# Performance work log

Measured on AMD Instinct MI355X. Metric: run time of the kernel, lower is better.

## Reference

```python
import jax, jax.numpy as jnp
import numpy as np

NUM_NODES = 200000
NUM_EDGES = 300000
NUM_QUERIES = 128
NUM_ENTITIES = 50000
N_DIMS = 256
N_DIMS_SM = 64
STATIC_DIM = 128
STATIC_SM = 32
G_IN = 2 * N_DIMS_SM + STATIC_SM + N_DIMS_SM  # 224


def leaky(x):
    return jnp.where(x > 0, x, 0.01 * x)


def setup_inputs() -> dict:
    key = jax.random.key(0)
    ks = jax.random.split(key, 24)
    W = 0.05  # weight scale to keep logits in a sane range
    inp = {
        'memorized_embedding': jax.random.normal(ks[0], (NUM_NODES, N_DIMS), jnp.float32),
        'node_score': jax.random.uniform(ks[1], (NUM_NODES,), jnp.float32),
        'rel_emb': jax.random.normal(ks[2], (NUM_EDGES, N_DIMS), jnp.float32),
        'query_src_ts_emb': jax.random.normal(ks[3], (NUM_QUERIES, STATIC_DIM), jnp.float32),
        'query_rel_emb': jax.random.normal(ks[4], (NUM_QUERIES, N_DIMS), jnp.float32),
        'eg_idx': jax.random.randint(ks[5], (NUM_EDGES,), 0, NUM_QUERIES, jnp.int32),
        'src_idx': jax.random.randint(ks[6], (NUM_EDGES,), 0, NUM_NODES, jnp.int32),
        'dst_idx': jax.random.randint(ks[7], (NUM_EDGES,), 0, NUM_NODES, jnp.int32),
        'entity_idx': jax.random.randint(ks[8], (NUM_NODES,), 0, NUM_ENTITIES, jnp.int32),
        'W_proj': W * jax.random.normal(ks[9], (N_DIMS, N_DIMS_SM), jnp.float32),
        'b_proj': W * jax.random.normal(ks[10], (N_DIMS_SM,), jnp.float32),
        'W_static': W * jax.random.normal(ks[11], (STATIC_DIM, STATIC_SM), jnp.float32),
        'b_static': W * jax.random.normal(ks[12], (STATIC_SM,), jnp.float32),
        'W_bs': W * jax.random.normal(ks[13], (N_DIMS, N_DIMS), jnp.float32),
        'b_bs': W * jax.random.normal(ks[14], (N_DIMS,), jnp.float32),
        'Wl': W * jax.random.normal(ks[15], (G_IN, N_DIMS_SM), jnp.float32),
        'bl': W * jax.random.normal(ks[16], (N_DIMS_SM,), jnp.float32),
        'Wr': W * jax.random.normal(ks[17], (G_IN, N_DIMS_SM), jnp.float32),
        'br': W * jax.random.normal(ks[18], (N_DIMS_SM,), jnp.float32),
        'Wc': W * jax.random.normal(ks[19], (N_DIMS_SM, N_DIMS_SM), jnp.float32),
        'bc': W * jax.random.normal(ks[20], (N_DIMS_SM,), jnp.float32),
    }
    return inp


def reference(memorized_embedding, node_score, rel_emb, query_src_ts_emb, query_rel_emb,
              eg_idx, src_idx, dst_idx, entity_idx,
              W_proj, b_proj, W_static, b_static, W_bs, b_bs,
              Wl, bl, Wr, br, Wc, bc):
    # one attention-flow step: linear_between_steps -> attention scoring (G) ->
    # per-source-node softmax -> attention propagation -> per-entity aggregation
    emb2 = leaky(memorized_embedding @ W_bs + b_bs)        # [N, d]
    # project all node embeddings once (linear commutes with gather)
    proj_all = emb2 @ W_proj + b_proj                       # [N, d_sm]
    hvi = proj_all[src_idx]                                 # [E, d_sm]
    hvj = proj_all[dst_idx]                                 # [E, d_sm]
    rel = rel_emb @ W_proj + b_proj                         # [E, d_sm]
    # context_dim_red
    qs = query_src_ts_emb @ W_static + b_static             # [B, static_sm]
    qr = query_rel_emb @ W_proj + b_proj                    # [B, d_sm]
    qs_e = qs[eg_idx]                                       # [E, static_sm]
    qr_e = qr[eg_idx]                                       # [E, d_sm]
    left = jnp.concatenate([hvi, rel, qs_e, qr_e], axis=-1)   # [E, G_IN]
    right = jnp.concatenate([hvj, rel, qs_e, qr_e], axis=-1)  # [E, G_IN]
    # G: sum(leaky(left W_l) * ((leaky(right W_r)) W_c))
    lh = leaky(left @ Wl + bl)                              # [E, d_sm]
    rh = leaky(right @ Wr + br) @ Wc + bc                   # [E, d_sm]
    logits = jnp.sum(lh * rh, axis=-1)                      # [E]
    # transition probability: softmax over outgoing edges of each source node
    seg_max = jax.ops.segment_max(logits, src_idx, num_segments=NUM_NODES)
    ex = jnp.exp(logits - seg_max[src_idx])
    denom = jax.ops.segment_sum(ex, src_idx, num_segments=NUM_NODES)
    trans = ex / denom[src_idx]
    # propagate node attention along edges (node_score_aggregation='sum')
    new_node_score = jax.ops.segment_sum(trans * node_score[src_idx], dst_idx,
                                         num_segments=NUM_NODES)
    # _aggregate_op_entity: sparse COO matmul == segment_sum over entity groups
    entity_att_score = jax.ops.segment_sum(new_node_score, entity_idx,
                                           num_segments=NUM_ENTITIES)
    return entity_att_score
```

## Files before the change

kernel.cpp:

```cpp
#include <hip/hip_runtime.h>
#include <hip/hip_bf16.h>

#define N_NODES 200000
#define N_EDGES 300000
#define N_Q     128
#define N_ENT   50000
#define D       256
#define DSM     64
#define SDIM    128
#define SSM     32

typedef __attribute__((ext_vector_type(8))) short bf16x8;
typedef __attribute__((ext_vector_type(4))) float f32x4;

__device__ __forceinline__ float leaky(float x){ return x > 0.f ? x : 0.01f*x; }

__device__ __forceinline__ unsigned short f2bf(float f){
  __hip_bfloat16 h = __float2bfloat16(f);
  return *reinterpret_cast<unsigned short*>(&h);
}
__device__ __forceinline__ unsigned pk2bf(float a, float b){
  float2 t; t.x = a; t.y = b;
  __hip_bfloat162 h = __float22bfloat162_rn(t);
  return *reinterpret_cast<unsigned*>(&h);
}
__device__ __forceinline__ float bf2f(unsigned short h){
  return __uint_as_float(((unsigned)h) << 16);
}

__device__ __forceinline__ void dev_pack(const float* __restrict__ src,
                                         unsigned short* __restrict__ dst,
                                         int K, int N, int id, int total){
  if (id >= total) return;
  int lane = id & 63, fb = id >> 6;
  int KB = K >> 5;
  int kb = fb % KB, nb = fb / KB;
  int k0 = kb*32 + ((lane>>4)<<3);
  int n  = nb*16 + (lane & 15);
  #pragma unroll
  for (int i = 0; i < 8; ++i) dst[(size_t)id*8 + i] = f2bf(src[(size_t)(k0+i)*N + n]);
}

__global__ void k_setup1(float* out, float* denom,
                         const float* __restrict__ Wp, const float* __restrict__ Wl,
                         const float* __restrict__ Wr, float* Wnlr, float* Wrlr,
                         const float* __restrict__ bp, float* cv,
                         const float* __restrict__ qsrc, const float* __restrict__ Ws,
                         const float* __restrict__ bs, const float* __restrict__ qrel,
                         float* qs, float* qr,
                         const float* __restrict__ Wbs, unsigned short* Wbs_pk,
                         const float* __restrict__ Wc, unsigned short* Wc_pk){
  int b = blockIdx.x, tid = threadIdx.x;
  if (b < 782){
    int id = b*256 + tid;
    if (id < N_ENT) out[id] = 0.f;
    if (id < N_NODES) denom[id] = 0.f;
  } else if (b < 1038){
    int id = (b-782)*256 + tid;
    int m = id >> 14, rem = id & 16383, k = rem >> 6, c = rem & 63;
    const float* Wsrc = (m & 1) ? Wr : Wl;
    int roff = (m >> 1) * 64;
    float s = 0.f;
    for (int i = 0; i < 64; ++i) s += Wp[k*64+i] * Wsrc[(roff+i)*64 + c];
    float* o = (m >> 1) ? Wrlr : Wnlr;
    o[k*128 + (m&1)*64 + c] = s;
  } else if (b == 1038){
    int m = tid >> 6, c = tid & 63;
    const float* Wsrc = (m & 1) ? Wr : Wl;
    int roff = (m >> 1) * 64;
    float s = 0.f;
    for (int i = 0; i < 64; ++i) s += bp[i] * Wsrc[(roff+i)*64 + c];
    cv[tid] = s;
  } else if (b < 1087){
    int id = (b-1039)*256 + tid;
    if (id < N_Q*SSM){
      int q = id >> 5, i = id & 31;
      float s = bs[i];
      for (int j = 0; j < SDIM; ++j) s += qsrc[q*SDIM+j] * Ws[j*SSM+i];
      qs[id] = s;
    } else {
      int id2 = id - N_Q*SSM;
      int q = id2 >> 6, i = id2 & 63;
      float s = bp[i];
      for (int j = 0; j < D; ++j) s += qrel[q*D+j] * Wp[j*DSM+i];
      qr[id2] = s;
    }
  } else if (b < 1119){
    dev_pack(Wbs, Wbs_pk, 256, 256, (b-1087)*256 + tid, 8192);
  } else {
    dev_pack(Wc, Wc_pk, 64, 64, (b-1119)*256 + tid, 512);
  }
}

__global__ void k_setup2(const float* __restrict__ qs, const float* __restrict__ qr,
                         const float* __restrict__ Wl, const float* __restrict__ bl,
                         const float* __restrict__ Wr, const float* __restrict__ br,
                         unsigned* qctx_p,
                         const float* __restrict__ Wnlr, unsigned short* Wn_pk,
                         const float* __restrict__ Wrlr, unsigned short* Wr_pk){
  int b = blockIdx.x, tid = threadIdx.x;
  if (b < 32){
    int id = b*256 + tid;
    int q = id >> 6, c = id & 63;
    float sl = bl[c], sr = br[c];
    for (int i = 0; i < SSM; ++i){
      float v = qs[q*SSM+i];
      sl += v * Wl[(128+i)*64+c];
      sr += v * Wr[(128+i)*64+c];
    }
    for (int i = 0; i < DSM; ++i){
      float v = qr[q*DSM+i];
      sl += v * Wl[(160+i)*64+c];
      sr += v * Wr[(160+i)*64+c];
    }
    qctx_p[id] = pk2bf(sl, sr);
  } else if (b < 48){
    dev_pack(Wnlr, Wn_pk, 256, 128, (b-32)*256 + tid, 4096);
  } else {
    dev_pack(Wrlr, Wr_pk, 256, 128, (b-48)*256 + tid, 4096);
  }
}

__global__ __launch_bounds__(256) void k_node(const float* __restrict__ A,
    const unsigned short* __restrict__ Wbs_pk, const float* __restrict__ bbs,
    const unsigned short* __restrict__ Wn_pk, const float* __restrict__ cv,
    unsigned short* __restrict__ node_l, unsigned short* __restrict__ node_r){
  __shared__ char smem[32768];
  int tid = threadIdx.x;
  int row0 = blockIdx.x * 64;
  {
    const float4* Ag = (const float4*)(A + (size_t)row0 * 256);
    #pragma unroll
    for (int it = 0; it < 16; ++it){
      int f = tid + 256*it;
      int r = f >> 6, c4 = f & 63;
      float4 v = Ag[f];
      uint2 u;
      u.x = pk2bf(v.x, v.y);
      u.y = pk2bf(v.z, v.w);
      int byte = (r << 9) + (c4 << 3);
      byte ^= (r & 7) << 4;
      *(uint2*)(smem + byte) = u;
    }
  }
  __syncthreads();
  int l = tid & 63, wn = tid >> 6;
  f32x4 acc[4][4];
  #pragma unroll
  for (int mf = 0; mf < 4; ++mf)
    #pragma unroll
    for (int nf = 0; nf < 4; ++nf) acc[mf][nf] = (f32x4){0.f,0.f,0.f,0.f};
  for (int kb = 0; kb < 8; ++kb){
    bf16x8 a[4], b[4];
    #pragma unroll
    for (int mf = 0; mf < 4; ++mf){
      int row = mf*16 + (l & 15);
      int byte = (row << 9) + kb*64 + ((l >> 4) << 4);
      byte ^= (row & 7) << 4;
      a[mf] = *(const bf16x8*)(smem + byte);
    }
    #pragma unroll
    for (int nf = 0; nf < 4; ++nf){
      int nb = wn*4 + nf;
      b[nf] = *(const bf16x8*)(Wbs_pk + ((size_t)(nb*8 + kb)*64 + l)*8);
    }
    #pragma unroll
    for (int mf = 0; mf < 4; ++mf)
      #pragma unroll
      for (int nf = 0; nf < 4; ++nf)
        acc[mf][nf] = __builtin_amdgcn_mfma_f32_16x16x32_bf16(a[mf], b[nf], acc[mf][nf], 0, 0, 0);
  }
  __syncthreads();
  #pragma unroll
  for (int mf = 0; mf < 4; ++mf)
    #pragma unroll
    for (int nf = 0; nf < 4; ++nf){
      int col = wn*64 + nf*16 + (l & 15);
      float bb = bbs[col];
      #pragma unroll
      for (int r = 0; r < 4; ++r){
        int row = mf*16 + ((l >> 4) << 2) + r;
        int byte = (row << 9) + col*2;
        byte ^= (row & 7) << 4;
        *(unsigned short*)(smem + byte) = f2bf(leaky(acc[mf][nf][r] + bb));
      }
    }
  __syncthreads();
  f32x4 acc2[4][2];
  #pragma unroll
  for (int mf = 0; mf < 4; ++mf){ acc2[mf][0] = (f32x4){0.f,0.f,0.f,0.f}; acc2[mf][1] = (f32x4){0.f,0.f,0.f,0.f}; }
  for (int kb = 0; kb < 8; ++kb){
    bf16x8 a[4], b[2];
    #pragma unroll
    for (int mf = 0; mf < 4; ++mf){
      int row = mf*16 + (l & 15);
      int byte = (row << 9) + kb*64 + ((l >> 4) << 4);
      byte ^= (row & 7) << 4;
      a[mf] = *(const bf16x8*)(smem + byte);
    }
    #pragma unroll
    for (int nf = 0; nf < 2; ++nf){
      int nb = wn*2 + nf;
      b[nf] = *(const bf16x8*)(Wn_pk + ((size_t)(nb*8 + kb)*64 + l)*8);
    }
    #pragma unroll
    for (int mf = 0; mf < 4; ++mf)
      #pragma unroll
      for (int nf = 0; nf < 2; ++nf)
        acc2[mf][nf] = __builtin_amdgcn_mfma_f32_16x16x32_bf16(a[mf], b[nf], acc2[mf][nf], 0, 0, 0);
  }
  #pragma unroll
  for (int mf = 0; mf < 4; ++mf)
    #pragma unroll
    for (int nf = 0; nf < 2; ++nf){
      int col = wn*32 + nf*16 + (l & 15);
      float cc = cv[col];
      #pragma unroll
      for (int r = 0; r < 4; ++r){
        int row = mf*16 + ((l >> 4) << 2) + r;
        unsigned short h = f2bf(acc2[mf][nf][r] + cc);
        size_t g = (size_t)(row0 + row);
        if (col < 64) node_l[g*64 + col] = h;
        else          node_r[g*64 + col - 64] = h;
      }
    }
}

__global__ __launch_bounds__(256) void k_rel(const float* __restrict__ relE,
    const unsigned short* __restrict__ Wr_pk, const float* __restrict__ cv,
    unsigned* __restrict__ rel_pk){
  __shared__ char smem[32768];
  int tid = threadIdx.x;
  int row0 = blockIdx.x * 64;
  {
    const float4* Rg = (const float4*)relE;
    #pragma unroll
    for (int it = 0; it < 16; ++it){
      int f = tid + 256*it;
      int r = f >> 6, c4 = f & 63;
      int ge = row0 + r; if (ge >= N_EDGES) ge = N_EDGES-1;
      float4 v = Rg[(size_t)ge*64 + c4];
      uint2 u;
      u.x = pk2bf(v.x, v.y);
      u.y = pk2bf(v.z, v.w);
      int byte = (r << 9) + (c4 << 3);
      byte ^= (r & 7) << 4;
      *(uint2*)(smem + byte) = u;
    }
  }
  __syncthreads();
  int l = tid & 63, wn = tid >> 6;
  f32x4 acc[4][2];
  #pragma unroll
  for (int mf = 0; mf < 4; ++mf){ acc[mf][0] = (f32x4){0.f,0.f,0.f,0.f}; acc[mf][1] = (f32x4){0.f,0.f,0.f,0.f}; }
  for (int kb = 0; kb < 8; ++kb){
    bf16x8 a[4], b0, b1;
    #pragma unroll
    for (int mf = 0; mf < 4; ++mf){
      int row = mf*16 + (l & 15);
      int byte = (row << 9) + kb*64 + ((l >> 4) << 4);
      byte ^= (row & 7) << 4;
      a[mf] = *(const bf16x8*)(smem + byte);
    }
    b0 = *(const bf16x8*)(Wr_pk + ((size_t)(wn*8 + kb)*64 + l)*8);
    b1 = *(const bf16x8*)(Wr_pk + ((size_t)((4+wn)*8 + kb)*64 + l)*8);
    #pragma unroll
    for (int mf = 0; mf < 4; ++mf){
      acc[mf][0] = __builtin_amdgcn_mfma_f32_16x16x32_bf16(a[mf], b0, acc[mf][0], 0, 0, 0);
      acc[mf][1] = __builtin_amdgcn_mfma_f32_16x16x32_bf16(a[mf], b1, acc[mf][1], 0, 0, 0);
    }
  }
  int c = wn*16 + (l & 15);
  float cvL = cv[128 + c], cvR = cv[192 + c];
  #pragma unroll
  for (int mf = 0; mf < 4; ++mf)
    #pragma unroll
    for (int r = 0; r < 4; ++r){
      int row = mf*16 + ((l >> 4) << 2) + r;
      int e = row0 + row;
      if (e < N_EDGES)
        rel_pk[(size_t)e*64 + c] = pk2bf(acc[mf][0][r] + cvL, acc[mf][1][r] + cvR);
    }
}

__global__ __launch_bounds__(256, 4) void k_score(const unsigned* __restrict__ rel_pk,
    const unsigned short* __restrict__ Wc_pk, const float* __restrict__ bc,
    const unsigned short* __restrict__ node_l, const unsigned short* __restrict__ node_r,
    const unsigned* __restrict__ qctx_p,
    const int* __restrict__ src, const int* __restrict__ dst, const int* __restrict__ eg,
    float* __restrict__ exbuf, float* __restrict__ denom){
  __shared__ char smem[16384];
  int tid = threadIdx.x;
  int l = tid & 63, wn = tid >> 6;
  char* wbase = smem + wn*4096;
  char* sLc  = wbase;
  char* sRin = wbase + 2048;
  int e0 = blockIdx.x * 64 + wn*16;

  int idxv;
  {
    int j = l & 15;
    int e = e0 + j;
    int ec = e < N_EDGES ? e : N_EDGES-1;
    const int* p = (l < 16) ? src : (l < 32) ? dst : eg;
    idxv = p[ec];
  }
  unsigned rlrv[16];
  unsigned short nlv[16], nrv[16];
  #pragma unroll
  for (int j = 0; j < 16; ++j){
    int e = e0 + j;
    int ec = e < N_EDGES ? e : N_EDGES-1;
    rlrv[j] = rel_pk[(size_t)ec*64 + l];
    int s  = __shfl(idxv, j);
    int d2 = __shfl(idxv, 16 + j);
    nlv[j] = node_l[(size_t)s*64 + l];
    nrv[j] = node_r[(size_t)d2*64 + l];
  }
  #pragma unroll
  for (int j = 0; j < 16; ++j){
    int e = e0 + j;
    int bL = (j << 7) + (l << 1);  bL ^= (j & 12) << 3;
    int bR = (j << 7) + (l << 1);  bR ^= (j & 7) << 4;
    unsigned short lh16 = 0, rr16 = 0;
    if (e < N_EDGES){
      int b = __shfl(idxv, 32 + j);
      unsigned qv = qctx_p[b*64 + l];
      unsigned rv = rlrv[j];
      float lh = leaky(bf2f(nlv[j]) + bf2f((unsigned short)(rv & 0xFFFFu))
                       + bf2f((unsigned short)(qv & 0xFFFFu)));
      float rr = leaky(bf2f(nrv[j]) + bf2f((unsigned short)(rv >> 16))
                       + bf2f((unsigned short)(qv >> 16)));
      lh16 = f2bf(lh); rr16 = f2bf(rr);
    }
    *(unsigned short*)(sLc + bL) = lh16;
    *(unsigned short*)(sRin + bR) = rr16;
  }
  float bcv[4];
  #pragma unroll
  for (int nf = 0; nf < 4; ++nf) bcv[nf] = bc[nf*16 + (l & 15)];
  f32x4 acc2[4];
  #pragma unroll
  for (int nf = 0; nf < 4; ++nf) acc2[nf] = (f32x4){0.f,0.f,0.f,0.f};
  #pragma unroll
  for (int kb = 0; kb < 2; ++kb){
    int row = l & 15;
    int byte = (row << 7) + kb*64 + ((l >> 4) << 4);
    byte ^= (row & 7) << 4;
    bf16x8 a = *(const bf16x8*)(sRin + byte);
    #pragma unroll
    for (int nf = 0; nf < 4; ++nf){
      bf16x8 bfr = *(const bf16x8*)(Wc_pk + ((size_t)(nf*2 + kb)*64 + l)*8);
      acc2[nf] = __builtin_amdgcn_mfma_f32_16x16x32_bf16(a, bfr, acc2[nf], 0, 0, 0);
    }
  }
  int srcj[4];
  float vr[4];
  #pragma unroll
  for (int r = 0; r < 4; ++r){
    int rowl = ((l >> 4) << 2) + r;
    srcj[r] = __shfl(idxv, rowl);
    float v = 0.f;
    #pragma unroll
    for (int nf = 0; nf < 4; ++nf){
      int col = nf*16 + (l & 15);
      int byte = (rowl << 7) + (col << 1);
      byte ^= (rowl & 12) << 3;
      v += (acc2[nf][r] + bcv[nf]) * bf2f(*(unsigned short*)(sLc + byte));
    }
    v += __shfl_xor(v, 1); v += __shfl_xor(v, 2);
    v += __shfl_xor(v, 4); v += __shfl_xor(v, 8);
    vr[r] = v;
  }
  if ((l & 15) == 0){
    #pragma unroll
    for (int r = 0; r < 4; ++r){
      int rowl = ((l >> 4) << 2) + r;
      int e = e0 + rowl;
      if (e < N_EDGES){
        float ex = __expf(vr[r]);
        exbuf[e] = ex;
        atomicAdd(&denom[srcj[r]], ex);
      }
    }
  }
}

__global__ void k_passC(const float* __restrict__ exbuf, const float* __restrict__ denom,
                        const int* __restrict__ src, const int* __restrict__ dst,
                        const float* __restrict__ node_score, const int* __restrict__ ent,
                        float* __restrict__ out){
  int e = blockIdx.x*256 + threadIdx.x;
  if (e >= N_EDGES) return;
  int s = src[e];
  float tr = exbuf[e] / denom[s];
  atomicAdd(&out[ent[dst[e]]], tr * node_score[s]);
}

extern "C" void kernel_launch(void* const* d_in, const int* in_sizes, int n_in,
                              void* d_out, int out_size, void* d_ws, size_t ws_size,
                              hipStream_t stream){
  const float* mem   = (const float*)d_in[0];
  const float* nsc   = (const float*)d_in[1];
  const float* relE  = (const float*)d_in[2];
  const float* qsrc  = (const float*)d_in[3];
  const float* qrel  = (const float*)d_in[4];
  const int*   eg    = (const int*)d_in[5];
  const int*   src   = (const int*)d_in[6];
  const int*   dst   = (const int*)d_in[7];
  const int*   ent   = (const int*)d_in[8];
  const float* Wp    = (const float*)d_in[9];
  const float* bp    = (const float*)d_in[10];
  const float* Ws    = (const float*)d_in[11];
  const float* bs    = (const float*)d_in[12];
  const float* Wbs   = (const float*)d_in[13];
  const float* bbs   = (const float*)d_in[14];
  const float* Wl    = (const float*)d_in[15];
  const float* bl    = (const float*)d_in[16];
  const float* Wr    = (const float*)d_in[17];
  const float* br    = (const float*)d_in[18];
  const float* Wc    = (const float*)d_in[19];
  const float* bc    = (const float*)d_in[20];
  float* out = (float*)d_out;

  char* w = (char*)d_ws;
  auto alloc = [&](size_t bytes)->void*{
    void* p = (void*)w; w += (bytes + 255) & ~(size_t)255; return p;
  };
  float* Wnlr = (float*)alloc(32768*4);
  float* Wrlr = (float*)alloc(32768*4);
  unsigned short* Wbs_pk = (unsigned short*)alloc(65536*2);
  unsigned short* Wn_pk  = (unsigned short*)alloc(32768*2);
  unsigned short* Wr_pk  = (unsigned short*)alloc(32768*2);
  unsigned short* Wc_pk  = (unsigned short*)alloc(4096*2);
  float* cv  = (float*)alloc(256*4);
  float* qs  = (float*)alloc((size_t)N_Q*SSM*4);
  float* qr  = (float*)alloc((size_t)N_Q*DSM*4);
  unsigned* qctx_p = (unsigned*)alloc((size_t)N_Q*DSM*4);
  unsigned short* node_l = (unsigned short*)alloc((size_t)N_NODES*64*2);
  unsigned short* node_r = (unsigned short*)alloc((size_t)N_NODES*64*2);
  unsigned* rel_pk = (unsigned*)alloc((size_t)N_EDGES*64*4);
  float* exbuf  = (float*)alloc((size_t)N_EDGES*4);
  float* denom = (float*)alloc((size_t)N_NODES*4);

  int egrid = (N_EDGES + 63) / 64;
  k_setup1<<<1121, 256, 0, stream>>>(out, denom,
                                     Wp, Wl, Wr, Wnlr, Wrlr, bp, cv,
                                     qsrc, Ws, bs, qrel, qs, qr,
                                     Wbs, Wbs_pk, Wc, Wc_pk);
  k_setup2<<<64, 256, 0, stream>>>(qs, qr, Wl, bl, Wr, br, qctx_p,
                                   Wnlr, Wn_pk, Wrlr, Wr_pk);
  k_rel<<<egrid, 256, 0, stream>>>(relE, Wr_pk, cv, rel_pk);
  k_node<<<N_NODES/64, 256, 0, stream>>>(mem, Wbs_pk, bbs, Wn_pk, cv, node_l, node_r);
  k_score<<<egrid, 256, 0, stream>>>(rel_pk, Wc_pk, bc, node_l, node_r, qctx_p,
                                     src, dst, eg, exbuf, denom);
  k_passC<<<(N_EDGES+255)/256, 256, 0, stream>>>(exbuf, denom, src, dst, nsc, ent, out);
}
```

Measured before the change: 277.1 us.

## Merge node and relation projection kernels into one interleaved launch

Fuses k_node and k_rel into a single k_proj kernel. Block indices are split 2:3 between node tiles and relation tiles, so the two streaming GEMM workloads run side by side and one launch and its tail drain are removed. The risk is higher register pressure, since the kernel now carries both code paths, and uneven per-block work across the mixed grid.

```diff
diff --git a/kernel.cpp b/kernel.cpp
--- a/kernel.cpp
+++ b/kernel.cpp
@@ -9,6 +9,9 @@
 #define DSM     64
 #define SDIM    128
 #define SSM     32
+
+#define NODE_BLKS 3125
+#define REL_BLKS  4688
 
 typedef __attribute__((ext_vector_type(8))) short bf16x8;
 typedef __attribute__((ext_vector_type(4))) float f32x4;
@@ -121,166 +124,169 @@
   }
 }
 
-__global__ __launch_bounds__(256) void k_node(const float* __restrict__ A,
+__global__ __launch_bounds__(256) void k_proj(const float* __restrict__ A,
     const unsigned short* __restrict__ Wbs_pk, const float* __restrict__ bbs,
     const unsigned short* __restrict__ Wn_pk, const float* __restrict__ cv,
-    unsigned short* __restrict__ node_l, unsigned short* __restrict__ node_r){
-  __shared__ char smem[32768];
-  int tid = threadIdx.x;
-  int row0 = blockIdx.x * 64;
-  {
-    const float4* Ag = (const float4*)(A + (size_t)row0 * 256);
-    #pragma unroll
-    for (int it = 0; it < 16; ++it){
-      int f = tid + 256*it;
-      int r = f >> 6, c4 = f & 63;
-      float4 v = Ag[f];
-      uint2 u;
-      u.x = pk2bf(v.x, v.y);
-      u.y = pk2bf(v.z, v.w);
-      int byte = (r << 9) + (c4 << 3);
-      byte ^= (r & 7) << 4;
-      *(uint2*)(smem + byte) = u;
-    }
-  }
-  __syncthreads();
-  int l = tid & 63, wn = tid >> 6;
-  f32x4 acc[4][4];
-  #pragma unroll
-  for (int mf = 0; mf < 4; ++mf)
-    #pragma unroll
-    for (int nf = 0; nf < 4; ++nf) acc[mf][nf] = (f32x4){0.f,0.f,0.f,0.f};
-  for (int kb = 0; kb < 8; ++kb){
-    bf16x8 a[4], b[4];
-    #pragma unroll
-    for (int mf = 0; mf < 4; ++mf){
-      int row = mf*16 + (l & 15);
-      int byte = (row << 9) + kb*64 + ((l >> 4) << 4);
-      byte ^= (row & 7) << 4;
-      a[mf] = *(const bf16x8*)(smem + byte);
-    }
-    #pragma unroll
-    for (int nf = 0; nf < 4; ++nf){
-      int nb = wn*4 + nf;
-      b[nf] = *(const bf16x8*)(Wbs_pk + ((size_t)(nb*8 + kb)*64 + l)*8);
-    }
-    #pragma unroll
-    for (int mf = 0; mf < 4; ++mf)
-      #pragma unroll
-      for (int nf = 0; nf < 4; ++nf)
-        acc[mf][nf] = __builtin_amdgcn_mfma_f32_16x16x32_bf16(a[mf], b[nf], acc[mf][nf], 0, 0, 0);
-  }
-  __syncthreads();
-  #pragma unroll
-  for (int mf = 0; mf < 4; ++mf)
-    #pragma unroll
-    for (int nf = 0; nf < 4; ++nf){
-      int col = wn*64 + nf*16 + (l & 15);
-      float bb = bbs[col];
-      #pragma unroll
-      for (int r = 0; r < 4; ++r){
-        int row = mf*16 + ((l >> 4) << 2) + r;
-        int byte = (row << 9) + col*2;
-        byte ^= (row & 7) << 4;
-        *(unsigned short*)(smem + byte) = f2bf(leaky(acc[mf][nf][r] + bb));
-      }
-    }
-  __syncthreads();
-  f32x4 acc2[4][2];
-  #pragma unroll
-  for (int mf = 0; mf < 4; ++mf){ acc2[mf][0] = (f32x4){0.f,0.f,0.f,0.f}; acc2[mf][1] = (f32x4){0.f,0.f,0.f,0.f}; }
-  for (int kb = 0; kb < 8; ++kb){
-    bf16x8 a[4], b[2];
-    #pragma unroll
-    for (int mf = 0; mf < 4; ++mf){
-      int row = mf*16 + (l & 15);
-      int byte = (row << 9) + kb*64 + ((l >> 4) << 4);
-      byte ^= (row & 7) << 4;
-      a[mf] = *(const bf16x8*)(smem + byte);
-    }
-    #pragma unroll
-    for (int nf = 0; nf < 2; ++nf){
-      int nb = wn*2 + nf;
-      b[nf] = *(const bf16x8*)(Wn_pk + ((size_t)(nb*8 + kb)*64 + l)*8);
-    }
-    #pragma unroll
-    for (int mf = 0; mf < 4; ++mf)
-      #pragma unroll
-      for (int nf = 0; nf < 2; ++nf)
-        acc2[mf][nf] = __builtin_amdgcn_mfma_f32_16x16x32_bf16(a[mf], b[nf], acc2[mf][nf], 0, 0, 0);
-  }
-  #pragma unroll
-  for (int mf = 0; mf < 4; ++mf)
-    #pragma unroll
-    for (int nf = 0; nf < 2; ++nf){
-      int col = wn*32 + nf*16 + (l & 15);
-      float cc = cv[col];
-      #pragma unroll
-      for (int r = 0; r < 4; ++r){
-        int row = mf*16 + ((l >> 4) << 2) + r;
-        unsigned short h = f2bf(acc2[mf][nf][r] + cc);
-        size_t g = (size_t)(row0 + row);
-        if (col < 64) node_l[g*64 + col] = h;
-        else          node_r[g*64 + col - 64] = h;
-      }
-    }
-}
-
-__global__ __launch_bounds__(256) void k_rel(const float* __restrict__ relE,
-    const unsigned short* __restrict__ Wr_pk, const float* __restrict__ cv,
+    unsigned short* __restrict__ node_l, unsigned short* __restrict__ node_r,
+    const float* __restrict__ relE, const unsigned short* __restrict__ Wr_pk,
     unsigned* __restrict__ rel_pk){
   __shared__ char smem[32768];
   int tid = threadIdx.x;
-  int row0 = blockIdx.x * 64;
-  {
-    const float4* Rg = (const float4*)relE;
-    #pragma unroll
-    for (int it = 0; it < 16; ++it){
-      int f = tid + 256*it;
-      int r = f >> 6, c4 = f & 63;
-      int ge = row0 + r; if (ge >= N_EDGES) ge = N_EDGES-1;
-      float4 v = Rg[(size_t)ge*64 + c4];
-      uint2 u;
-      u.x = pk2bf(v.x, v.y);
-      u.y = pk2bf(v.z, v.w);
-      int byte = (r << 9) + (c4 << 3);
-      byte ^= (r & 7) << 4;
-      *(uint2*)(smem + byte) = u;
-    }
-  }
-  __syncthreads();
   int l = tid & 63, wn = tid >> 6;
-  f32x4 acc[4][2];
-  #pragma unroll
-  for (int mf = 0; mf < 4; ++mf){ acc[mf][0] = (f32x4){0.f,0.f,0.f,0.f}; acc[mf][1] = (f32x4){0.f,0.f,0.f,0.f}; }
-  for (int kb = 0; kb < 8; ++kb){
-    bf16x8 a[4], b0, b1;
-    #pragma unroll
-    for (int mf = 0; mf < 4; ++mf){
-      int row = mf*16 + (l & 15);
-      int byte = (row << 9) + kb*64 + ((l >> 4) << 4);
-      byte ^= (row & 7) << 4;
-      a[mf] = *(const bf16x8*)(smem + byte);
-    }
-    b0 = *(const bf16x8*)(Wr_pk + ((size_t)(wn*8 + kb)*64 + l)*8);
-    b1 = *(const bf16x8*)(Wr_pk + ((size_t)((4+wn)*8 + kb)*64 + l)*8);
-    #pragma unroll
-    for (int mf = 0; mf < 4; ++mf){
-      acc[mf][0] = __builtin_amdgcn_mfma_f32_16x16x32_bf16(a[mf], b0, acc[mf][0], 0, 0, 0);
-      acc[mf][1] = __builtin_amdgcn_mfma_f32_16x16x32_bf16(a[mf], b1, acc[mf][1], 0, 0, 0);
-    }
-  }
-  int c = wn*16 + (l & 15);
-  float cvL = cv[128 + c], cvR = cv[192 + c];
-  #pragma unroll
-  for (int mf = 0; mf < 4; ++mf)
-    #pragma unroll
-    for (int r = 0; r < 4; ++r){
-      int row = mf*16 + ((l >> 4) << 2) + r;
-      int e = row0 + row;
-      if (e < N_EDGES)
-        rel_pk[(size_t)e*64 + c] = pk2bf(acc[mf][0][r] + cvL, acc[mf][1][r] + cvR);
-    }
+  int g = blockIdx.x / 5, r5 = blockIdx.x % 5;
+
+  if (r5 < 2){
+    int nb = g*2 + r5;
+    if (nb >= NODE_BLKS) return;
+    int row0 = nb * 64;
+    {
+      const float4* Ag = (const float4*)(A + (size_t)row0 * 256);
+      #pragma unroll
+      for (int it = 0; it < 16; ++it){
+        int f = tid + 256*it;
+        int r = f >> 6, c4 = f & 63;
+        float4 v = Ag[f];
+        uint2 u;
+        u.x = pk2bf(v.x, v.y);
+        u.y = pk2bf(v.z, v.w);
+        int byte = (r << 9) + (c4 << 3);
+        byte ^= (r & 7) << 4;
+        *(uint2*)(smem + byte) = u;
+      }
+    }
+    __syncthreads();
+    f32x4 acc[4][4];
+    #pragma unroll
+    for (int mf = 0; mf < 4; ++mf)
+      #pragma unroll
+      for (int nf = 0; nf < 4; ++nf) acc[mf][nf] = (f32x4){0.f,0.f,0.f,0.f};
+    for (int kb = 0; kb < 8; ++kb){
+      bf16x8 a[4], b[4];
+      #pragma unroll
+      for (int mf = 0; mf < 4; ++mf){
+        int row = mf*16 + (l & 15);
+        int byte = (row << 9) + kb*64 + ((l >> 4) << 4);
+        byte ^= (row & 7) << 4;
+        a[mf] = *(const bf16x8*)(smem + byte);
+      }
+      #pragma unroll
+      for (int nf = 0; nf < 4; ++nf){
+        int nbb = wn*4 + nf;
+        b[nf] = *(const bf16x8*)(Wbs_pk + ((size_t)(nbb*8 + kb)*64 + l)*8);
+      }
+      #pragma unroll
+      for (int mf = 0; mf < 4; ++mf)
+        #pragma unroll
+        for (int nf = 0; nf < 4; ++nf)
+          acc[mf][nf] = __builtin_amdgcn_mfma_f32_16x16x32_bf16(a[mf], b[nf], acc[mf][nf], 0, 0, 0);
+    }
+    __syncthreads();
+    #pragma unroll
+    for (int mf = 0; mf < 4; ++mf)
+      #pragma unroll
+      for (int nf = 0; nf < 4; ++nf){
+        int col = wn*64 + nf*16 + (l & 15);
+        float bb = bbs[col];
+        #pragma unroll
+        for (int r = 0; r < 4; ++r){
+          int row = mf*16 + ((l >> 4) << 2) + r;
+          int byte = (row << 9) + col*2;
+          byte ^= (row & 7) << 4;
+          *(unsigned short*)(smem + byte) = f2bf(leaky(acc[mf][nf][r] + bb));
+        }
+      }
+    __syncthreads();
+    f32x4 acc2[4][2];
+    #pragma unroll
+    for (int mf = 0; mf < 4; ++mf){ acc2[mf][0] = (f32x4){0.f,0.f,0.f,0.f}; acc2[mf][1] = (f32x4){0.f,0.f,0.f,0.f}; }
+    for (int kb = 0; kb < 8; ++kb){
+      bf16x8 a[4], b[2];
+      #pragma unroll
+      for (int mf = 0; mf < 4; ++mf){
+        int row = mf*16 + (l & 15);
+        int byte = (row << 9) + kb*64 + ((l >> 4) << 4);
+        byte ^= (row & 7) << 4;
+        a[mf] = *(const bf16x8*)(smem + byte);
+      }
+      #pragma unroll
+      for (int nf = 0; nf < 2; ++nf){
+        int nbb = wn*2 + nf;
+        b[nf] = *(const bf16x8*)(Wn_pk + ((size_t)(nbb*8 + kb)*64 + l)*8);
+      }
+      #pragma unroll
+      for (int mf = 0; mf < 4; ++mf)
+        #pragma unroll
+        for (int nf = 0; nf < 2; ++nf)
+          acc2[mf][nf] = __builtin_amdgcn_mfma_f32_16x16x32_bf16(a[mf], b[nf], acc2[mf][nf], 0, 0, 0);
+    }
+    #pragma unroll
+    for (int mf = 0; mf < 4; ++mf)
+      #pragma unroll
+      for (int nf = 0; nf < 2; ++nf){
+        int col = wn*32 + nf*16 + (l & 15);
+        float cc = cv[col];
+        #pragma unroll
+        for (int r = 0; r < 4; ++r){
+          int row = mf*16 + ((l >> 4) << 2) + r;
+          unsigned short h = f2bf(acc2[mf][nf][r] + cc);
+          size_t gg = (size_t)(row0 + row);
+          if (col < 64) node_l[gg*64 + col] = h;
+          else          node_r[gg*64 + col - 64] = h;
+        }
+      }
+  } else {
+    int rb = g*3 + (r5 - 2);
+    if (rb >= REL_BLKS) return;
+    int row0 = rb * 64;
+    {
+      const float4* Rg = (const float4*)relE;
+      #pragma unroll
+      for (int it = 0; it < 16; ++it){
+        int f = tid + 256*it;
+        int r = f >> 6, c4 = f & 63;
+        int ge = row0 + r; if (ge >= N_EDGES) ge = N_EDGES-1;
+        float4 v = Rg[(size_t)ge*64 + c4];
+        uint2 u;
+        u.x = pk2bf(v.x, v.y);
+        u.y = pk2bf(v.z, v.w);
+        int byte = (r << 9) + (c4 << 3);
+        byte ^= (r & 7) << 4;
+        *(uint2*)(smem + byte) = u;
+      }
+    }
+    __syncthreads();
+    f32x4 acc[4][2];
+    #pragma unroll
+    for (int mf = 0; mf < 4; ++mf){ acc[mf][0] = (f32x4){0.f,0.f,0.f,0.f}; acc[mf][1] = (f32x4){0.f,0.f,0.f,0.f}; }
+    for (int kb = 0; kb < 8; ++kb){
+      bf16x8 a[4], b0, b1;
+      #pragma unroll
+      for (int mf = 0; mf < 4; ++mf){
+        int row = mf*16 + (l & 15);
+        int byte = (row << 9) + kb*64 + ((l >> 4) << 4);
+        byte ^= (row & 7) << 4;
+        a[mf] = *(const bf16x8*)(smem + byte);
+      }
+      b0 = *(const bf16x8*)(Wr_pk + ((size_t)(wn*8 + kb)*64 + l)*8);
+      b1 = *(const bf16x8*)(Wr_pk + ((size_t)((4+wn)*8 + kb)*64 + l)*8);
+      #pragma unroll
+      for (int mf = 0; mf < 4; ++mf){
+        acc[mf][0] = __builtin_amdgcn_mfma_f32_16x16x32_bf16(a[mf], b0, acc[mf][0], 0, 0, 0);
+        acc[mf][1] = __builtin_amdgcn_mfma_f32_16x16x32_bf16(a[mf], b1, acc[mf][1], 0, 0, 0);
+      }
+    }
+    int c = wn*16 + (l & 15);
+    float cvL = cv[128 + c], cvR = cv[192 + c];
+    #pragma unroll
+    for (int mf = 0; mf < 4; ++mf)
+      #pragma unroll
+      for (int r = 0; r < 4; ++r){
+        int row = mf*16 + ((l >> 4) << 2) + r;
+        int e = row0 + row;
+        if (e < N_EDGES)
+          rel_pk[(size_t)e*64 + c] = pk2bf(acc[mf][0][r] + cvL, acc[mf][1][r] + cvR);
+      }
+  }
 }
 
 __global__ __launch_bounds__(256, 4) void k_score(const unsigned* __restrict__ rel_pk,
@@ -443,16 +449,15 @@
   float* exbuf  = (float*)alloc((size_t)N_EDGES*4);
   float* denom = (float*)alloc((size_t)N_NODES*4);
 
-  int egrid = (N_EDGES + 63) / 64;
   k_setup1<<<1121, 256, 0, stream>>>(out, denom,
                                      Wp, Wl, Wr, Wnlr, Wrlr, bp, cv,
                                      qsrc, Ws, bs, qrel, qs, qr,
                                      Wbs, Wbs_pk, Wc, Wc_pk);
   k_setup2<<<64, 256, 0, stream>>>(qs, qr, Wl, bl, Wr, br, qctx_p,
                                    Wnlr, Wn_pk, Wrlr, Wr_pk);
-  k_rel<<<egrid, 256, 0, stream>>>(relE, Wr_pk, cv, rel_pk);
-  k_node<<<N_NODES/64, 256, 0, stream>>>(mem, Wbs_pk, bbs, Wn_pk, cv, node_l, node_r);
-  k_score<<<egrid, 256, 0, stream>>>(rel_pk, Wc_pk, bc, node_l, node_r, qctx_p,
-                                     src, dst, eg, exbuf, denom);
+  k_proj<<<1563*5, 256, 0, stream>>>(mem, Wbs_pk, bbs, Wn_pk, cv, node_l, node_r,
+                                     relE, Wr_pk, rel_pk);
+  k_score<<<(N_EDGES+63)/64, 256, 0, stream>>>(rel_pk, Wc_pk, bc, node_l, node_r, qctx_p,
+                                               src, dst, eg, exbuf, denom);
   k_passC<<<(N_EDGES+255)/256, 256, 0, stream>>>(exbuf, denom, src, dst, nsc, ent, out);
 }
```

Measured after the change: 231.2 us (median of 2 runs). 1.2x faster.
